# Kernel tuning notes

Hardware: AMD Instinct MI355X
Metric: run time of the kernel (lower is better)

Reference implementation:

```python
import jax, jax.numpy as jnp
import numpy as np

B, S, E, H = 2, 2048, 1024, 16
D = E // H

def setup_inputs() -> dict:
    key = jax.random.key(0)
    ks = jax.random.split(key, 5)
    return {
        "hidden_states": jax.random.normal(ks[0], (B, S, E), dtype=jnp.float32),
        "c_attn_w": jax.random.normal(ks[1], (E, 3 * E), dtype=jnp.float32) * 0.02,
        "c_attn_b": jax.random.normal(ks[2], (3 * E,), dtype=jnp.float32) * 0.02,
        "c_proj_w": jax.random.normal(ks[3], (E, E), dtype=jnp.float32) * 0.02,
        "c_proj_b": jax.random.normal(ks[4], (E,), dtype=jnp.float32) * 0.02,
    }

def reference(hidden_states, c_attn_w, c_attn_b, c_proj_w, c_proj_b):
    x = hidden_states                      # [B, S, E]
    b, s, _ = x.shape
    w_q, w_k, w_v = jnp.split(c_attn_w, 3, axis=1)   # each [E, E]
    q_b, k_b, v_b = jnp.split(c_attn_b, 3, axis=0)   # each [E]

    # value projection
    v = x @ w_v + v_b                                        # [B,S,E]
    v = v.reshape(b, s, H, D).transpose(0, 2, 1, 3)          # [B,H,S,D]

    # fused query: ((x Wq + qb) Wk^T + kb)
    q = (x @ w_q + q_b) @ w_k.T + k_b                        # [B,S,E]
    qh = q.reshape(b, s, H, D).transpose(0, 2, 1, 3)         # [B,H,S,D]

    # key side is RAW hidden states split per head
    kh = x.reshape(b, s, H, D).transpose(0, 2, 1, 3)         # [B,H,S,D]

    scale = 1.0 / jnp.float32(D) ** 0.5
    scores = jnp.einsum("bhqd,bhkd->bhqk",
                        qh.astype(jnp.float32),
                        kh.astype(jnp.float32)) * scale       # [B,H,S,S] fp32

    causal = jnp.tril(jnp.ones((s, s), dtype=bool))
    mask_value = jnp.finfo(jnp.float32).min
    scores = jnp.where(causal[None, None], scores, mask_value)

    probs = jax.nn.softmax(scores, axis=-1).astype(v.dtype)  # [B,H,S,S]

    out = jnp.einsum("bhqk,bhkd->bhqd", probs, v)            # [B,H,S,D]
    out = out.transpose(0, 2, 1, 3).reshape(b, s, E)         # [B,S,E]
    out = out @ c_proj_w + c_proj_b
    return out
```

## Files before the change

### kernel.cpp

```cpp
#include <hip/hip_runtime.h>

typedef __attribute__((ext_vector_type(8))) __bf16 bf16x8;
typedef __attribute__((ext_vector_type(4))) __bf16 bf16x4;
typedef __attribute__((ext_vector_type(4))) float f32x4;

typedef __attribute__((address_space(1))) void as1_void;
typedef __attribute__((address_space(3))) void as3_void;

__device__ __forceinline__ void gl_lds16(const void* g, void* l) {
    __builtin_amdgcn_global_load_lds((const as1_void*)g, (as3_void*)l, 16, 0, 0);
}

__device__ __forceinline__ const bf16x8* swz(const __bf16* base, int row, int chunk) {
    return (const bf16x8*)((const char*)base + row * 128 + ((chunk ^ (row & 7)) * 16));
}

#define QSCALE (0.125f * 1.44269504f)

__global__ __launch_bounds__(256) void prep_kernel(
    const float* __restrict__ x, const float* __restrict__ caw,
    const float* __restrict__ cpw,
    __bf16* __restrict__ xb, __bf16* __restrict__ wvt,
    __bf16* __restrict__ wpt, __bf16* __restrict__ wqt,
    __bf16* __restrict__ wkn)
{
    __shared__ float tile[32 * 33];
    int bid = blockIdx.x;
    int tid = threadIdx.x;
    if (bid < 1024) {
        int nt = bid >> 5, kt = bid & 31;
        int tx = tid & 31, ty = tid >> 5;
        int n0 = nt * 32, k0 = kt * 32;
#pragma unroll
        for (int i = 0; i < 4; ++i)
            tile[(ty + i * 8) * 33 + tx] = caw[(long)(k0 + ty + i * 8) * 3072 + 2048 + n0 + tx];
        __syncthreads();
#pragma unroll
        for (int i = 0; i < 4; ++i)
            wvt[(long)(n0 + ty + i * 8) * 1024 + k0 + tx] = (__bf16)tile[tx * 33 + ty + i * 8];
    } else if (bid < 2048) {
        int v = bid - 1024;
        int nt = v >> 5, kt = v & 31;
        int tx = tid & 31, ty = tid >> 5;
        int n0 = nt * 32, k0 = kt * 32;
#pragma unroll
        for (int i = 0; i < 4; ++i)
            tile[(ty + i * 8) * 33 + tx] = cpw[(long)(k0 + ty + i * 8) * 1024 + n0 + tx];
        __syncthreads();
#pragma unroll
        for (int i = 0; i < 4; ++i)
            wpt[(long)(n0 + ty + i * 8) * 1024 + k0 + tx] = (__bf16)tile[tx * 33 + ty + i * 8];
    } else if (bid < 3072) {
        int v = bid - 2048;
        int nt = v >> 5, kt = v & 31;
        int tx = tid & 31, ty = tid >> 5;
        int n0 = nt * 32, k0 = kt * 32;
#pragma unroll
        for (int i = 0; i < 4; ++i)
            tile[(ty + i * 8) * 33 + tx] = caw[(long)(k0 + ty + i * 8) * 3072 + n0 + tx];
        __syncthreads();
#pragma unroll
        for (int i = 0; i < 4; ++i)
            wqt[(long)(n0 + ty + i * 8) * 1024 + k0 + tx] = (__bf16)tile[tx * 33 + ty + i * 8];
    } else if (bid < 4096) {
        int e = (bid - 3072) * 1024 + tid * 4;
        int n = e >> 10, k = e & 1023;
        float4 f = *(const float4*)(caw + (long)n * 3072 + 1024 + k);
        bf16x4 o = {(__bf16)f.x, (__bf16)f.y, (__bf16)f.z, (__bf16)f.w};
        *(bf16x4*)(wkn + e) = o;
    } else {
        long e = (long)(bid - 4096) * 1024 + tid * 4;
        float4 f = *(const float4*)(x + e);
        bf16x4 o = {(__bf16)f.x, (__bf16)f.y, (__bf16)f.z, (__bf16)f.w};
        *(bf16x4*)(xb + e) = o;
    }
}

__global__ __launch_bounds__(256) void gemm_tv(
    const __bf16* __restrict__ xb, const __bf16* __restrict__ wqt,
    const __bf16* __restrict__ wvt, const float* __restrict__ cab,
    __bf16* __restrict__ tb, __bf16* __restrict__ vt)
{
    __shared__ __bf16 smem[128 * 136];
    const int bid = blockIdx.x;
    const int tid = threadIdx.x;
    const int lane = tid & 63;
    const int wave = tid >> 6;
    const int quad = lane >> 4, l16 = lane & 15;

    if (bid < 512) {
        __bf16* As = smem;
        __bf16* Bs = smem + 8192;
        const int bx = bid & 15, by = bid >> 4;
        const long m0 = (long)by * 128;
        const long n0 = (long)bx * 64;
        const int wm = (wave >> 1) * 64, wn = (wave & 1) * 32;

        f32x4 acc[4][2] = {};
        for (int k0 = 0; k0 < 1024; k0 += 64) {
#pragma unroll
            for (int c = tid; c < 1536; c += 256) {
                int row = c >> 3, cc = (c & 7) ^ (row & 7);
                if (row < 128)
                    gl_lds16(xb + (m0 + row) * 1024 + k0 + cc * 8, As + c * 8);
                else
                    gl_lds16(wqt + (n0 + row - 128) * 1024 + k0 + cc * 8, Bs + (c - 1024) * 8);
            }
            __syncthreads();
#pragma unroll
            for (int kk = 0; kk < 2; ++kk) {
                bf16x8 af[4], bfr[2];
#pragma unroll
                for (int i = 0; i < 4; ++i)
                    af[i] = *swz(As, wm + i * 16 + l16, kk * 4 + quad);
#pragma unroll
                for (int j = 0; j < 2; ++j)
                    bfr[j] = *swz(Bs, wn + j * 16 + l16, kk * 4 + quad);
#pragma unroll
                for (int i = 0; i < 4; ++i)
#pragma unroll
                    for (int j = 0; j < 2; ++j)
                        acc[i][j] = __builtin_amdgcn_mfma_f32_16x16x32_bf16(af[i], bfr[j], acc[i][j], 0, 0, 0);
            }
            __syncthreads();
        }
#pragma unroll
        for (int i = 0; i < 4; ++i) {
            long row = m0 + wm + i * 16 + quad * 4;
#pragma unroll
            for (int j = 0; j < 2; ++j) {
                int col = (int)n0 + wn + j * 16 + l16;
                float bb = cab[col];
#pragma unroll
                for (int r = 0; r < 4; ++r)
                    tb[(row + r) * 1024 + col] = (__bf16)(acc[i][j][r] + bb);
            }
        }
    } else {
        __bf16* As = smem;
        __bf16* Bs = smem + 8192;
        const int v2 = bid - 512;
        const int bx = v2 & 7, by = v2 >> 3;
        const long m0 = (long)by * 128;
        const long n0 = (long)bx * 128;
        const int wm = (wave >> 1) * 64, wn = (wave & 1) * 64;

        f32x4 acc[4][4] = {};
        for (int k0 = 0; k0 < 1024; k0 += 64) {
#pragma unroll
            for (int c = tid; c < 2048; c += 256) {
                int row = c >> 3, cc = (c & 7) ^ (row & 7);
                if (row < 128)
                    gl_lds16(xb + (m0 + row) * 1024 + k0 + cc * 8, As + c * 8);
                else
                    gl_lds16(wvt + (n0 + row - 128) * 1024 + k0 + cc * 8, Bs + (c - 1024) * 8);
            }
            __syncthreads();
#pragma unroll
            for (int kk = 0; kk < 2; ++kk) {
                bf16x8 af[4], bfr[4];
#pragma unroll
                for (int i = 0; i < 4; ++i)
                    af[i] = *swz(As, wm + i * 16 + l16, kk * 4 + quad);
#pragma unroll
                for (int j = 0; j < 4; ++j)
                    bfr[j] = *swz(Bs, wn + j * 16 + l16, kk * 4 + quad);
#pragma unroll
                for (int i = 0; i < 4; ++i)
#pragma unroll
                    for (int j = 0; j < 4; ++j)
                        acc[i][j] = __builtin_amdgcn_mfma_f32_16x16x32_bf16(af[i], bfr[j], acc[i][j], 0, 0, 0);
            }
            __syncthreads();
        }
        __syncthreads();
#pragma unroll
        for (int i = 0; i < 4; ++i) {
#pragma unroll
            for (int j = 0; j < 4; ++j) {
                int col = (int)n0 + wn + j * 16 + l16;
                float bb = cab[2048 + col];
                bf16x4 v;
#pragma unroll
                for (int r = 0; r < 4; ++r) v[r] = (__bf16)(acc[i][j][r] + bb);
                *(bf16x4*)(smem + (wn + j * 16 + l16) * 136 + wm + i * 16 + quad * 4) = v;
            }
        }
        __syncthreads();
        const int bb2 = (int)(m0 >> 11);
        const int sl = (int)(m0 & 2047);
#pragma unroll
        for (int pass = 0; pass < 16; ++pass) {
            int idx = pass * 256 + tid;
            int n = idx >> 5;
            int mc = (idx & 31) * 4;
            bf16x4 v = *(const bf16x4*)(smem + n * 136 + mc);
            *(bf16x4*)(vt + ((long)(bb2 * 1024 + (int)n0 + n)) * 2048 + sl + mc) = v;
        }
    }
}

__global__ __launch_bounds__(512) void attn_kernel(
    const __bf16* __restrict__ T,
    const __bf16* __restrict__ Xb,
    const __bf16* __restrict__ VT,
    const __bf16* __restrict__ WK,
    const float* __restrict__ cab,
    __bf16* __restrict__ O)
{
    __shared__ __bf16 Ks[2 * 8192];
    __shared__ __bf16 Vs[2 * 8192];
    __shared__ __bf16 Ps[8 * 1024];
    const int tid = threadIdx.x;
    const int lane = tid & 63;
    const int wave = tid >> 6;
    const int group = wave >> 2;
    const int w4 = wave & 3;
    const int quad = lane >> 4, l16 = lane & 15;
    const int qa = blockIdx.y;
    const int qb = 31 - qa;
    const int qt = group ? qb : qa;
    const int bh = blockIdx.x;
    const int b = bh >> 4, h = bh & 15;
    const long rowbase = (long)b * 2048;

    const int s0 = tid;
    const int c0 = ((s0 & 7) ^ ((s0 >> 3) & 7)) * 8;

    bf16x8 ones;
#pragma unroll
    for (int i = 0; i < 8; ++i) ones[i] = (__bf16)1.0f;

    bf16x8 qfr[2];
    {
        f32x4 qacc[4] = {};
        for (int k0 = 0; k0 < 1024; k0 += 64) {
#pragma unroll
            for (int u = 0; u < 3; ++u) {
                int c = tid + u * 512;
                if (c < 1024) {
                    int lr = c >> 3;
                    int cc = (c & 7) ^ (lr & 7);
                    int grow = (lr < 64) ? qa * 64 + lr : qb * 64 + (lr - 64);
                    gl_lds16(T + (rowbase + grow) * 1024 + k0 + cc * 8, Ks + c * 8);
                } else {
                    int w = c - 1024;
                    int lr = w >> 3;
                    int cc = (w & 7) ^ (lr & 7);
                    gl_lds16(WK + (long)(h * 64 + lr) * 1024 + k0 + cc * 8, Vs + w * 8);
                }
            }
            __syncthreads();
#pragma unroll
            for (int kk = 0; kk < 2; ++kk) {
                bf16x8 af = *swz(Ks + group * 4096, w4 * 16 + l16, kk * 4 + quad);
#pragma unroll
                for (int dt = 0; dt < 4; ++dt) {
                    bf16x8 bfr = *swz(Vs, dt * 16 + l16, kk * 4 + quad);
                    qacc[dt] = __builtin_amdgcn_mfma_f32_16x16x32_bf16(af, bfr, qacc[dt], 0, 0, 0);
                }
            }
            __syncthreads();
        }
#pragma unroll
        for (int dt = 0; dt < 4; ++dt) {
            int d = dt * 16 + l16;
            float bb = cab[1024 + h * 64 + d];
#pragma unroll
            for (int r = 0; r < 4; ++r) {
                int row = group * 64 + w4 * 16 + quad * 4 + r;
                float v = (qacc[dt][r] + bb) * QSCALE;
                *(__bf16*)((char*)Ps + row * 128 + (((d >> 3) ^ (row & 7)) * 16) + (d & 7) * 2) = (__bf16)v;
            }
        }
        __syncthreads();
        qfr[0] = *swz(Ps + group * 4096, w4 * 16 + l16, quad);
        qfr[1] = *swz(Ps + group * 4096, w4 * 16 + l16, 4 + quad);
    }

    const __bf16* kp0 = Xb + (rowbase + (s0 >> 3)) * 1024 + h * 64 + c0;
    const __bf16* vp0 = VT + ((long)(b * 1024 + h * 64 + (s0 >> 3))) * 2048 + c0;

    auto stage_tile = [&](int j, int buf, int sub) {
        gl_lds16(kp0 + (long)j * 65536, Ks + buf * 8192 + sub * 4096 + s0 * 8);
        gl_lds16(vp0 + j * 64, Vs + buf * 8192 + sub * 4096 + s0 * 8);
    };
    stage_tile(0, 0, 0);
    stage_tile(1, 0, 1);

    const int nouter = (qb + 2) >> 1;

    f32x4 oacc[4] = {};
    f32x4 lacc = {};
    __bf16* Pw = Ps + wave * 1024;

    for (int jj = 0; jj < nouter; ++jj) {
        __syncthreads();
        if (jj + 1 < nouter) {
            stage_tile(2 * jj + 2, (jj + 1) & 1, 0);
            stage_tile(2 * jj + 3, (jj + 1) & 1, 1);
        }

#pragma unroll
        for (int sub = 0; sub < 2; ++sub) {
            const int j = 2 * jj + sub;
            if (j > qt) continue;
            const __bf16* Kb = Ks + (jj & 1) * 8192 + sub * 4096;
            const __bf16* Vb = Vs + (jj & 1) * 8192 + sub * 4096;

            bf16x8 kf[2][4], vf[2][4];
#pragma unroll
            for (int kk = 0; kk < 2; ++kk)
#pragma unroll
                for (int kt = 0; kt < 4; ++kt) {
                    kf[kk][kt] = *swz(Kb, kt * 16 + l16, kk * 4 + quad);
                    vf[kk][kt] = *swz(Vb, kt * 16 + l16, kk * 4 + quad);
                }

            f32x4 sacc[4] = {};
            __builtin_amdgcn_s_setprio(1);
#pragma unroll
            for (int kk = 0; kk < 2; ++kk)
#pragma unroll
                for (int kt = 0; kt < 4; ++kt)
                    sacc[kt] = __builtin_amdgcn_mfma_f32_16x16x32_bf16(
                        kf[kk][kt], qfr[kk], sacc[kt], 0, 0, 0);
            __builtin_amdgcn_s_setprio(0);

            if (j == qt) {
                const int qloc = w4 * 16 + l16;
#pragma unroll
                for (int kt = 0; kt < 4; ++kt) {
                    bf16x4 pk;
#pragma unroll
                    for (int r = 0; r < 4; ++r) {
                        float s = sacc[kt][r];
                        if (kt * 16 + quad * 4 + r > qloc) s = -1e30f;
                        pk[r] = (__bf16)exp2f(s);
                    }
                    *(bf16x4*)((char*)Pw + l16 * 128 +
                               (((kt * 2 + (quad >> 1)) ^ (l16 & 7)) * 16) + (quad & 1) * 8) = pk;
                }
            } else {
#pragma unroll
                for (int kt = 0; kt < 4; ++kt) {
                    bf16x4 pk;
#pragma unroll
                    for (int r = 0; r < 4; ++r)
                        pk[r] = (__bf16)exp2f(sacc[kt][r]);
                    *(bf16x4*)((char*)Pw + l16 * 128 +
                               (((kt * 2 + (quad >> 1)) ^ (l16 & 7)) * 16) + (quad & 1) * 8) = pk;
                }
            }

            __builtin_amdgcn_s_setprio(1);
#pragma unroll
            for (int kk = 0; kk < 2; ++kk) {
                bf16x8 pf = *swz(Pw, l16, kk * 4 + quad);
                lacc = __builtin_amdgcn_mfma_f32_16x16x32_bf16(ones, pf, lacc, 0, 0, 0);
#pragma unroll
                for (int dt = 0; dt < 4; ++dt)
                    oacc[dt] = __builtin_amdgcn_mfma_f32_16x16x32_bf16(
                        vf[kk][dt], pf, oacc[dt], 0, 0, 0);
            }
            __builtin_amdgcn_s_setprio(0);
        }
    }

    {
        float inv = 1.0f / lacc[0];
        long row = rowbase + qt * 64 + w4 * 16 + l16;
#pragma unroll
        for (int dt = 0; dt < 4; ++dt) {
            bf16x4 ov;
#pragma unroll
            for (int r = 0; r < 4; ++r) ov[r] = (__bf16)(oacc[dt][r] * inv);
            *(bf16x4*)(O + row * 1024 + h * 64 + dt * 16 + quad * 4) = ov;
        }
    }
}

__global__ __launch_bounds__(256) void gemm_proj(
    const __bf16* __restrict__ A, const __bf16* __restrict__ B,
    const float* __restrict__ bias, float* __restrict__ C)
{
    __shared__ __bf16 As[128 * 64];
    __shared__ __bf16 Bs[64 * 64];
    const int tid = threadIdx.x;
    const int lane = tid & 63;
    const int wave = tid >> 6;
    const int quad = lane >> 4, l16 = lane & 15;
    const long m0 = (long)blockIdx.y * 128;
    const long n0 = (long)blockIdx.x * 64;
    const int wm = (wave >> 1) * 64, wn = (wave & 1) * 32;

    f32x4 acc[4][2] = {};

    for (int k0 = 0; k0 < 1024; k0 += 64) {
#pragma unroll
        for (int c = tid; c < 1536; c += 256) {
            int row = c >> 3, cc = (c & 7) ^ (row & 7);
            if (row < 128)
                gl_lds16(A + (m0 + row) * 1024 + k0 + cc * 8, As + c * 8);
            else
                gl_lds16(B + (n0 + row - 128) * 1024 + k0 + cc * 8, Bs + (c - 1024) * 8);
        }
        __syncthreads();
#pragma unroll
        for (int kk = 0; kk < 2; ++kk) {
            bf16x8 af[4], bfr[2];
#pragma unroll
            for (int i = 0; i < 4; ++i)
                af[i] = *swz(As, wm + i * 16 + l16, kk * 4 + quad);
#pragma unroll
            for (int j = 0; j < 2; ++j)
                bfr[j] = *swz(Bs, wn + j * 16 + l16, kk * 4 + quad);
#pragma unroll
            for (int i = 0; i < 4; ++i)
#pragma unroll
                for (int j = 0; j < 2; ++j)
                    acc[i][j] = __builtin_amdgcn_mfma_f32_16x16x32_bf16(af[i], bfr[j], acc[i][j], 0, 0, 0);
        }
        __syncthreads();
    }
#pragma unroll
    for (int i = 0; i < 4; ++i) {
        long row = m0 + wm + i * 16 + quad * 4;
#pragma unroll
        for (int j = 0; j < 2; ++j) {
            int col = (int)n0 + wn + j * 16 + l16;
            float bb = bias[col];
#pragma unroll
            for (int r = 0; r < 4; ++r)
                C[(row + r) * 1024 + col] = acc[i][j][r] + bb;
        }
    }
}

extern "C" void kernel_launch(void* const* d_in, const int* in_sizes, int n_in,
                              void* d_out, int out_size, void* d_ws, size_t ws_size,
                              hipStream_t stream) {
    const float* x   = (const float*)d_in[0];
    const float* caw = (const float*)d_in[1];
    const float* cab = (const float*)d_in[2];
    const float* cpw = (const float*)d_in[3];
    const float* cpb = (const float*)d_in[4];

    char* p = (char*)d_ws;
    auto alloc = [&](size_t bytes) {
        void* r = (void*)p;
        p += (bytes + 255) & ~(size_t)255;
        return r;
    };
    __bf16* xb    = (__bf16*)alloc(4096UL * 1024 * 2);
    __bf16* wkn   = (__bf16*)alloc(1024UL * 1024 * 2);
    __bf16* wvt   = (__bf16*)alloc(1024UL * 1024 * 2);
    __bf16* wqt   = (__bf16*)alloc(1024UL * 1024 * 2);
    __bf16* wpt   = (__bf16*)alloc(1024UL * 1024 * 2);
    __bf16* tb    = (__bf16*)alloc(4096UL * 1024 * 2);
    __bf16* abuf  = (__bf16*)alloc(4096UL * 1024 * 2);
    __bf16* vt    = (__bf16*)alloc(2048UL * 2048 * 2);

    prep_kernel<<<8192, 256, 0, stream>>>(x, caw, cpw, xb, wvt, wpt, wqt, wkn);
    gemm_tv<<<768, 256, 0, stream>>>(xb, wqt, wvt, cab, tb, vt);
    attn_kernel<<<dim3(32, 16), 512, 0, stream>>>(tb, xb, vt, wkn, cab, abuf);
    gemm_proj<<<dim3(16, 32), 256, 0, stream>>>(abuf, wpt, cpb, (float*)d_out);
    (void)in_sizes; (void)n_in; (void)out_size; (void)ws_size;
}
```

Measured before the change: 174.9 us.

## Triple-buffer the in-kernel Q projection prologue with async LDS loads

The per-block query projection loop in the attention kernel now prefetches the next K-slice of T and WK into one of three rotating LDS buffers while computing on the current one. It waits with a partial vmcnt and a single barrier per iteration instead of two full __syncthreads, so global-to-LDS latency overlaps the MFMA work. Shared memory is merged into one array with the buffers carved out of it. The third B buffer overlaps the Ps region, which relies on the final-iteration barrier for safety.

```diff
diff --git a/kernel.cpp b/kernel.cpp
--- a/kernel.cpp
+++ b/kernel.cpp
@@ -208,9 +208,10 @@
     const float* __restrict__ cab,
     __bf16* __restrict__ O)
 {
-    __shared__ __bf16 Ks[2 * 8192];
-    __shared__ __bf16 Vs[2 * 8192];
-    __shared__ __bf16 Ps[8 * 1024];
+    __shared__ __bf16 SM[40960];
+    __bf16* Ks = SM;
+    __bf16* Vs = SM + 16384;
+    __bf16* Ps = SM + 32768;
     const int tid = threadIdx.x;
     const int lane = tid & 63;
     const int wave = tid >> 6;
@@ -233,8 +234,9 @@
 
     bf16x8 qfr[2];
     {
-        f32x4 qacc[4] = {};
-        for (int k0 = 0; k0 < 1024; k0 += 64) {
+        auto stage_q = [&](int ki, int buf) {
+            __bf16* Ad = SM + buf * 8192;
+            __bf16* Bd = SM + 24576 + buf * 4096;
 #pragma unroll
             for (int u = 0; u < 3; ++u) {
                 int c = tid + u * 512;
@@ -242,25 +244,38 @@
                     int lr = c >> 3;
                     int cc = (c & 7) ^ (lr & 7);
                     int grow = (lr < 64) ? qa * 64 + lr : qb * 64 + (lr - 64);
-                    gl_lds16(T + (rowbase + grow) * 1024 + k0 + cc * 8, Ks + c * 8);
+                    gl_lds16(T + (rowbase + grow) * 1024 + ki * 64 + cc * 8, Ad + c * 8);
                 } else {
                     int w = c - 1024;
                     int lr = w >> 3;
                     int cc = (w & 7) ^ (lr & 7);
-                    gl_lds16(WK + (long)(h * 64 + lr) * 1024 + k0 + cc * 8, Vs + w * 8);
+                    gl_lds16(WK + (long)(h * 64 + lr) * 1024 + ki * 64 + cc * 8, Bd + w * 8);
                 }
             }
-            __syncthreads();
+        };
+
+        f32x4 qacc[4] = {};
+        stage_q(0, 0);
+        for (int ki = 0; ki < 16; ++ki) {
+            if (ki < 15) {
+                stage_q(ki + 1, (ki + 1) % 3);
+                asm volatile("s_waitcnt vmcnt(3)" ::: "memory");
+            } else {
+                asm volatile("s_waitcnt vmcnt(0)" ::: "memory");
+            }
+            __builtin_amdgcn_sched_barrier(0);
+            __builtin_amdgcn_s_barrier();
+            const __bf16* Aq = SM + (ki % 3) * 8192;
+            const __bf16* Bq = SM + 24576 + (ki % 3) * 4096;
 #pragma unroll
             for (int kk = 0; kk < 2; ++kk) {
-                bf16x8 af = *swz(Ks + group * 4096, w4 * 16 + l16, kk * 4 + quad);
+                bf16x8 af = *swz(Aq + group * 4096, w4 * 16 + l16, kk * 4 + quad);
 #pragma unroll
                 for (int dt = 0; dt < 4; ++dt) {
-                    bf16x8 bfr = *swz(Vs, dt * 16 + l16, kk * 4 + quad);
+                    bf16x8 bfr = *swz(Bq, dt * 16 + l16, kk * 4 + quad);
                     qacc[dt] = __builtin_amdgcn_mfma_f32_16x16x32_bf16(af, bfr, qacc[dt], 0, 0, 0);
                 }
             }
-            __syncthreads();
         }
 #pragma unroll
         for (int dt = 0; dt < 4; ++dt) {
```

Result: slower. 181.1 us (+3.6%).
